# Kernel optimization log

Measured on AMD Instinct MI355X. Metric: run time of the kernel, lower is better.

Reference implementation:

```python
import jax, jax.numpy as jnp
import numpy as np
import math

B, M, N = 1, 128, 256
LIG_C = 256      # rep_1d num_c
ATTN_C = 32      # attention_num_c
HEADS = 8        # num_heads
EPS = 1e-5


def setup_inputs() -> dict:
    key = jax.random.key(0)
    ks = jax.random.split(key, 8)
    s = 1.0 / math.sqrt(LIG_C)
    return {
        "lig_profile": jax.random.normal(ks[0], (B, M, N, LIG_C), dtype=jnp.float32),
        "ln_scale": jnp.ones((LIG_C,), dtype=jnp.float32),
        "ln_bias": jnp.zeros((LIG_C,), dtype=jnp.float32),
        "wq": jax.random.normal(ks[1], (LIG_C, ATTN_C * HEADS), dtype=jnp.float32) * s,
        "wk": jax.random.normal(ks[2], (LIG_C, ATTN_C * HEADS), dtype=jnp.float32) * s,
        "wv": jax.random.normal(ks[3], (LIG_C, ATTN_C * HEADS), dtype=jnp.float32) * s,
        "wf": jax.random.normal(ks[4], (ATTN_C * HEADS, LIG_C), dtype=jnp.float32) * s,
        "bf": jnp.zeros((LIG_C,), dtype=jnp.float32),
    }


def reference(lig_profile, ln_scale, ln_bias, wq, wk, wv, wf, bf):
    # LayerNorm over channel dim
    mu = jnp.mean(lig_profile, axis=-1, keepdims=True)
    var = jnp.mean(jnp.square(lig_profile - mu), axis=-1, keepdims=True)
    x = (lig_profile - mu) * jax.lax.rsqrt(var + EPS) * ln_scale + ln_bias

    # QKV projections; view splits last dim as (attn_c, heads) -> channel-major layout
    shape5 = x.shape[:-1] + (ATTN_C, HEADS)
    q = (x @ wq).reshape(shape5)  # [b,m,n,c,h]
    k = (x @ wk).reshape(shape5)
    v = (x @ wv).reshape(shape5)

    factor = 1.0 / math.sqrt(ATTN_C)
    aff = jnp.einsum('bmich,bmjch->bmijh', q, k) * factor  # [b,m,i,j,h]
    weights = jax.nn.softmax(aff, axis=-2)                  # softmax over j (keys)
    out = jnp.einsum('bmrch,bmirh->bmich', v, weights)      # [b,m,i,c,h]
    out = out.reshape(out.shape[:-2] + (ATTN_C * HEADS,))
    return out @ wf + bf
```

## Files before the change

kernel.cpp:

```cpp
#include <hip/hip_runtime.h>

typedef _Float16 f16;
typedef _Float16 f16x8 __attribute__((ext_vector_type(8)));
typedef _Float16 f16x4 __attribute__((ext_vector_type(4)));
typedef _Float16 f16x2 __attribute__((ext_vector_type(2)));
typedef float f32x4 __attribute__((ext_vector_type(4)));
typedef float f32x16 __attribute__((ext_vector_type(16)));

#define MDIM 128
#define NDIM 256
#define CDIM 256
#define ROWS (MDIM*NDIM)

__device__ inline int pk2(float a, float b) {
  union { f16x2 h; int i; } u;
  u.h[0] = (f16)a; u.h[1] = (f16)b;
  return u.i;
}

__global__ __launch_bounds__(256) void k_prep(
    const float* __restrict__ wq, const float* __restrict__ wk,
    const float* __restrict__ wv, const float* __restrict__ wf,
    f16* __restrict__ bq, f16* __restrict__ bk, f16* __restrict__ bv,
    f16* __restrict__ bw)
{
  int idx   = blockIdx.x & 255;
  int which = blockIdx.x >> 8;
  int kk    = threadIdx.x;
  if (which < 3) {
    const float* W = which == 0 ? wq : which == 1 ? wk : wv;
    f16* dst       = which == 0 ? bq : which == 1 ? bk : bv;
    float sc = which == 0 ? (0.17677669529663689f * 1.4426950408889634f) : 1.0f;
    int j = (idx & 31) * 8 + (idx >> 5);
    dst[idx * 256 + kk] = (f16)(W[(size_t)kk * 256 + j] * sc);
  } else {
    int pkk = (kk & 31) * 8 + (kk >> 5);
    bw[idx * 256 + kk] = (f16)wf[(size_t)pkk * 256 + idx];
  }
}

__global__ __launch_bounds__(256) void k_lnqkv(const float* __restrict__ x,
    const float* __restrict__ g, const float* __restrict__ bb,
    const f16* __restrict__ bq, const f16* __restrict__ bk, const f16* __restrict__ bv,
    f16* __restrict__ qo, f16* __restrict__ ko, f16* __restrict__ vT)
{
  __shared__ f16 As[64][264];
  __shared__ f16 Bs[64][264];
  __shared__ f16 vtmp[64][72];
  int bm = blockIdx.x;
  int t = threadIdx.x, lane = t & 63, w = t >> 6;
  int wr = w >> 1, wc = w & 1;
  int l15 = lane & 15, l4 = lane >> 4;
  const float4 gv  = *(const float4*)(g + lane * 4);
  const float4 bv4 = *(const float4*)(bb + lane * 4);
#pragma unroll 4
  for (int rr = 0; rr < 16; ++rr) {
    int r = w * 16 + rr;
    const float4 xv = *(const float4*)(x + (size_t)(bm * 64 + r) * 256 + lane * 4);
    float s  = xv.x + xv.y + xv.z + xv.w;
    float s2 = xv.x*xv.x + xv.y*xv.y + xv.z*xv.z + xv.w*xv.w;
#pragma unroll
    for (int mm = 1; mm < 64; mm <<= 1) {
      s  += __shfl_xor(s,  mm, 64);
      s2 += __shfl_xor(s2, mm, 64);
    }
    float mu  = s * (1.0f / 256.0f);
    float var = s2 * (1.0f / 256.0f) - mu * mu;
    float rs  = rsqrtf(var + 1e-5f);
    f16x4 ov;
    ov[0] = (f16)((xv.x - mu) * rs * gv.x + bv4.x);
    ov[1] = (f16)((xv.y - mu) * rs * gv.y + bv4.y);
    ov[2] = (f16)((xv.z - mu) * rs * gv.z + bv4.z);
    ov[3] = (f16)((xv.w - mu) * rs * gv.w + bv4.w);
    *(f16x4*)&As[r][lane * 4] = ov;
  }
  for (int ct = 0; ct < 12; ++ct) {
    const f16* B = ct < 4 ? bq : ct < 8 ? bk : bv;
    int je0 = (ct & 3) * 64;
#pragma unroll
    for (int p = 0; p < 8; ++p) {
      int r = t >> 2, c0 = (t & 3) * 8 + p * 32;
      *(f16x8*)&Bs[r][c0] = *(const f16x8*)(B + (size_t)(je0 + r) * 256 + c0);
    }
    __syncthreads();
    f32x4 acc[2][2] = {};
#pragma unroll
    for (int kt = 0; kt < 8; ++kt) {
      f16x8 a0 = *(const f16x8*)&As[wr * 32 +      l15][kt * 32 + l4 * 8];
      f16x8 a1 = *(const f16x8*)&As[wr * 32 + 16 + l15][kt * 32 + l4 * 8];
      f16x8 b0 = *(const f16x8*)&Bs[wc * 32 +      l15][kt * 32 + l4 * 8];
      f16x8 b1 = *(const f16x8*)&Bs[wc * 32 + 16 + l15][kt * 32 + l4 * 8];
      acc[0][0] = __builtin_amdgcn_mfma_f32_16x16x32_f16(a0, b0, acc[0][0], 0, 0, 0);
      acc[0][1] = __builtin_amdgcn_mfma_f32_16x16x32_f16(a0, b1, acc[0][1], 0, 0, 0);
      acc[1][0] = __builtin_amdgcn_mfma_f32_16x16x32_f16(a1, b0, acc[1][0], 0, 0, 0);
      acc[1][1] = __builtin_amdgcn_mfma_f32_16x16x32_f16(a1, b1, acc[1][1], 0, 0, 0);
    }
    if (ct < 8) {
      f16* dst = ct < 4 ? qo : ko;
#pragma unroll
      for (int mi = 0; mi < 2; ++mi)
#pragma unroll
        for (int ni = 0; ni < 2; ++ni)
#pragma unroll
          for (int r = 0; r < 4; ++r) {
            int row = bm * 64 + wr * 32 + mi * 16 + l4 * 4 + r;
            int col = je0 + wc * 32 + ni * 16 + l15;
            dst[(size_t)row * 256 + col] = (f16)acc[mi][ni][r];
          }
    } else {
#pragma unroll
      for (int mi = 0; mi < 2; ++mi)
#pragma unroll
        for (int ni = 0; ni < 2; ++ni)
#pragma unroll
          for (int r = 0; r < 4; ++r)
            vtmp[wc * 32 + ni * 16 + l15][wr * 32 + mi * 16 + l4 * 4 + r] = (f16)acc[mi][ni][r];
      __syncthreads();
      int ch = t >> 2, np = (t & 3) * 16;
      size_t gdst = ((size_t)(bm >> 2) * 256 + je0 + ch) * 256 + (bm & 3) * 64 + np;
      *(f16x8*)(vT + gdst)     = *(const f16x8*)&vtmp[ch][np];
      *(f16x8*)(vT + gdst + 8) = *(const f16x8*)&vtmp[ch][np + 8];
    }
    __syncthreads();
  }
}

__global__ __launch_bounds__(256, 4) void k_attn(const f16* __restrict__ q,
    const f16* __restrict__ k, const f16* __restrict__ vT, f16* __restrict__ o)
{
  __shared__ f16 ks[256][40];
  __shared__ f16 vt[32][264];
  int bx = blockIdx.x;
  int m = bx >> 4, h = (bx >> 1) & 7, half = bx & 1;
  int t = threadIdx.x, lane = t & 63, w = t >> 6;
  int i32 = lane & 31, hi = lane >> 5;
  size_t rowbase = (size_t)m * 256;
#pragma unroll
  for (int p = 0; p < 4; ++p) {
    int n = p * 64 + (t >> 2);
    int c0 = (t & 3) * 8;
    *(f16x8*)&ks[n][c0] = *(const f16x8*)(k + (rowbase + n) * 256 + h * 32 + c0);
  }
#pragma unroll
  for (int p = 0; p < 4; ++p) {
    int idx = p * 256 + t;
    int c = idx >> 5, nb = (idx & 31) * 8;
    *(f16x8*)&vt[c][nb] = *(const f16x8*)(vT + ((size_t)m * 256 + h * 32 + c) * 256 + nb);
  }
  __syncthreads();
  int qi0 = half * 128 + w * 32;
  const f16* qp = q + (rowbase + qi0 + i32) * 256 + h * 32 + hi * 8;
  f16x8 qf0 = *(const f16x8*)(qp);
  f16x8 qf1 = *(const f16x8*)(qp + 16);
  f32x16 O = {};
  float m_run = -1e30f, l_run = 0.f;
#pragma unroll 2
  for (int kb = 0; kb < 8; ++kb) {
    f16x8 kf0 = *(const f16x8*)&ks[kb * 32 + i32][hi * 8];
    f16x8 kf1 = *(const f16x8*)&ks[kb * 32 + i32][16 + hi * 8];
    f32x16 s = {};
    s = __builtin_amdgcn_mfma_f32_32x32x16_f16(kf0, qf0, s, 0, 0, 0);
    s = __builtin_amdgcn_mfma_f32_32x32x16_f16(kf1, qf1, s, 0, 0, 0);
    float pmax = s[0];
#pragma unroll
    for (int r = 1; r < 16; ++r) pmax = fmaxf(pmax, s[r]);
    pmax = fmaxf(pmax, __shfl_xor(pmax, 32, 64));
    if (!__all(pmax - m_run <= 8.f)) {
      float m_new = fmaxf(m_run, pmax);
      float f = __builtin_amdgcn_exp2f(m_run - m_new);
      l_run *= f;
#pragma unroll
      for (int r = 0; r < 16; ++r)
        O[r] *= __shfl(f, (r & 3) + 8 * (r >> 2) + 4 * hi, 64);
      m_run = m_new;
    }
    float lsum = 0.f;
#pragma unroll
    for (int r = 0; r < 16; ++r) {
      float e = __builtin_amdgcn_exp2f(s[r] - m_run);
      s[r] = e;
      lsum += e;
    }
    lsum += __shfl_xor(lsum, 32, 64);
    l_run += lsum;
    int W0[4], W1[4];
#pragma unroll
    for (int qq = 0; qq < 4; ++qq) {
      W0[qq] = pk2(s[4 * qq],     s[4 * qq + 1]);
      W1[qq] = pk2(s[4 * qq + 2], s[4 * qq + 3]);
    }
#pragma unroll
    for (int ks2 = 0; ks2 < 2; ++ks2) {
      int X0 = W0[2 * ks2], Y0 = W0[2 * ks2 + 1];
      int X1 = W1[2 * ks2], Y1 = W1[2 * ks2 + 1];
      int a0 = __shfl(X0, i32, 64),      b0 = __shfl(Y0, i32, 64);
      int a1 = __shfl(X1, i32, 64),      b1 = __shfl(Y1, i32, 64);
      int a2 = __shfl(X0, i32 + 32, 64), b2 = __shfl(Y0, i32 + 32, 64);
      int a3 = __shfl(X1, i32 + 32, 64), b3 = __shfl(Y1, i32 + 32, 64);
      union { unsigned int ww[4]; f16x8 v; } pa;
      pa.ww[0] = hi ? (unsigned)b0 : (unsigned)a0;
      pa.ww[1] = hi ? (unsigned)b1 : (unsigned)a1;
      pa.ww[2] = hi ? (unsigned)b2 : (unsigned)a2;
      pa.ww[3] = hi ? (unsigned)b3 : (unsigned)a3;
      f16x8 vb = *(const f16x8*)&vt[i32][kb * 32 + ks2 * 16 + hi * 8];
      O = __builtin_amdgcn_mfma_f32_32x32x16_f16(pa.v, vb, O, 0, 0, 0);
    }
  }
  float inv = 1.f / l_run;
#pragma unroll
  for (int r = 0; r < 16; ++r) {
    int i = (r & 3) + 8 * (r >> 2) + 4 * hi;
    float fr = __shfl(inv, i, 64);
    o[(rowbase + (size_t)(qi0 + i)) * 256 + h * 32 + i32] = (f16)(O[r] * fr);
  }
}

__global__ __launch_bounds__(256) void k_out(const f16* __restrict__ a,
    const f16* __restrict__ bw, const float* __restrict__ bias,
    float* __restrict__ out)
{
  __shared__ f16 As[64][264];
  __shared__ f16 Bs[64][264];
  int bm = blockIdx.x;
  int t = threadIdx.x, lane = t & 63, w = t >> 6;
  int wr = w >> 1, wc = w & 1;
  int l15 = lane & 15, l4 = lane >> 4;
#pragma unroll
  for (int p = 0; p < 8; ++p) {
    int r = t >> 2, c0 = (t & 3) * 8 + p * 32;
    *(f16x8*)&As[r][c0] = *(const f16x8*)(a + (size_t)(bm * 64 + r) * 256 + c0);
  }
  for (int ct = 0; ct < 4; ++ct) {
    int col0 = ct * 64;
#pragma unroll
    for (int p = 0; p < 8; ++p) {
      int r = t >> 2, c0 = (t & 3) * 8 + p * 32;
      *(f16x8*)&Bs[r][c0] = *(const f16x8*)(bw + (size_t)(col0 + r) * 256 + c0);
    }
    __syncthreads();
    f32x4 acc[2][2] = {};
#pragma unroll
    for (int kt = 0; kt < 8; ++kt) {
      f16x8 a0 = *(const f16x8*)&As[wr * 32 +      l15][kt * 32 + l4 * 8];
      f16x8 a1 = *(const f16x8*)&As[wr * 32 + 16 + l15][kt * 32 + l4 * 8];
      f16x8 b0 = *(const f16x8*)&Bs[wc * 32 +      l15][kt * 32 + l4 * 8];
      f16x8 b1 = *(const f16x8*)&Bs[wc * 32 + 16 + l15][kt * 32 + l4 * 8];
      acc[0][0] = __builtin_amdgcn_mfma_f32_16x16x32_f16(a0, b0, acc[0][0], 0, 0, 0);
      acc[0][1] = __builtin_amdgcn_mfma_f32_16x16x32_f16(a0, b1, acc[0][1], 0, 0, 0);
      acc[1][0] = __builtin_amdgcn_mfma_f32_16x16x32_f16(a1, b0, acc[1][0], 0, 0, 0);
      acc[1][1] = __builtin_amdgcn_mfma_f32_16x16x32_f16(a1, b1, acc[1][1], 0, 0, 0);
    }
#pragma unroll
    for (int mi = 0; mi < 2; ++mi)
#pragma unroll
      for (int ni = 0; ni < 2; ++ni)
#pragma unroll
        for (int r = 0; r < 4; ++r) {
          int row = bm * 64 + wr * 32 + mi * 16 + l4 * 4 + r;
          int col = col0 + wc * 32 + ni * 16 + l15;
          out[(size_t)row * 256 + col] = acc[mi][ni][r] + bias[col];
        }
    __syncthreads();
  }
}

extern "C" void kernel_launch(void* const* d_in, const int* in_sizes, int n_in,
                              void* d_out, int out_size, void* d_ws, size_t ws_size,
                              hipStream_t stream)
{
  const float* x  = (const float*)d_in[0];
  const float* g  = (const float*)d_in[1];
  const float* b  = (const float*)d_in[2];
  const float* wq = (const float*)d_in[3];
  const float* wk = (const float*)d_in[4];
  const float* wv = (const float*)d_in[5];
  const float* wf = (const float*)d_in[6];
  const float* bf = (const float*)d_in[7];
  float* out = (float*)d_out;

  char* ws = (char*)d_ws;
  f16* ah  = (f16*)(ws);
  f16* qh  = (f16*)(ws + (size_t)16 * 1024 * 1024);
  f16* kh  = (f16*)(ws + (size_t)32 * 1024 * 1024);
  f16* vTh = (f16*)(ws + (size_t)48 * 1024 * 1024);
  char* wbase = ws + (size_t)64 * 1024 * 1024;
  f16* bq = (f16*)(wbase);
  f16* bk = (f16*)(wbase + 128 * 1024);
  f16* bv = (f16*)(wbase + 256 * 1024);
  f16* bw = (f16*)(wbase + 384 * 1024);

  k_prep <<<1024, 256, 0, stream>>>(wq, wk, wv, wf, bq, bk, bv, bw);
  k_lnqkv<<<512,  256, 0, stream>>>(x, g, b, bq, bk, bv, qh, kh, vTh);
  k_attn <<<2048, 256, 0, stream>>>(qh, kh, vTh, ah);
  k_out  <<<512,  256, 0, stream>>>(ah, bw, bf, out);
}
```

Measured before the change: 84.05 us.

## Prefetch GEMM weight tiles, merge attention halves, add MFMA priority, coalesce weight prep

The weight-prep kernel now transposes through LDS with coalesced reads and vectorized writes, using only 16 blocks. The QKV and output GEMMs register-prefetch the next weight tile while the current one is computed. Attention merges the two query halves into one 512-thread block so K/V are loaded once per (m,h), and wraps the MFMAs with s_setprio. The log2e factor moves from the Q weights to a per-score multiply. These are meant to cut redundant K/V loads and hide global-load latency, at the cost of extra VALU work and more register pressure. A 16-block prep kernel also leaves most CUs idle.

```diff
diff --git a/kernel.cpp b/kernel.cpp
--- a/kernel.cpp
+++ b/kernel.cpp
@@ -11,6 +11,7 @@
 #define NDIM 256
 #define CDIM 256
 #define ROWS (MDIM*NDIM)
+#define L2E 1.4426950408889634f
 
 __device__ inline int pk2(float a, float b) {
   union { f16x2 h; int i; } u;
@@ -24,18 +25,39 @@
     f16* __restrict__ bq, f16* __restrict__ bk, f16* __restrict__ bv,
     f16* __restrict__ bw)
 {
-  int idx   = blockIdx.x & 255;
-  int which = blockIdx.x >> 8;
-  int kk    = threadIdx.x;
+  __shared__ f16 ld[64][264];
+  int which = blockIdx.x >> 2, kb = blockIdx.x & 3;
+  int t = threadIdx.x;
+  int k0 = kb * 64;
   if (which < 3) {
     const float* W = which == 0 ? wq : which == 1 ? wk : wv;
     f16* dst       = which == 0 ? bq : which == 1 ? bk : bv;
-    float sc = which == 0 ? (0.17677669529663689f * 1.4426950408889634f) : 1.0f;
-    int j = (idx & 31) * 8 + (idx >> 5);
-    dst[idx * 256 + kk] = (f16)(W[(size_t)kk * 256 + j] * sc);
+    float sc = which == 0 ? 0.17677669529663689f : 1.0f;
+    for (int r = 0; r < 64; ++r)
+      ld[r][t] = (f16)(W[(size_t)(k0 + r) * 256 + t] * sc);
+    __syncthreads();
+    int j = (t & 31) * 8 + (t >> 5);
+#pragma unroll
+    for (int rr = 0; rr < 8; ++rr) {
+      f16x8 o;
+#pragma unroll
+      for (int i = 0; i < 8; ++i) o[i] = ld[rr * 8 + i][j];
+      *(f16x8*)(dst + (size_t)t * 256 + k0 + rr * 8) = o;
+    }
   } else {
-    int pkk = (kk & 31) * 8 + (kk >> 5);
-    bw[idx * 256 + kk] = (f16)wf[(size_t)pkk * 256 + idx];
+    for (int r = 0; r < 64; ++r) {
+      int ke = k0 + r;
+      int jr = (ke & 31) * 8 + (ke >> 5);
+      ld[r][t] = (f16)wf[(size_t)jr * 256 + t];
+    }
+    __syncthreads();
+#pragma unroll
+    for (int rr = 0; rr < 8; ++rr) {
+      f16x8 o;
+#pragma unroll
+      for (int i = 0; i < 8; ++i) o[i] = ld[rr * 8 + i][t];
+      *(f16x8*)(bw + (size_t)t * 256 + k0 + rr * 8) = o;
+    }
   }
 }
 
@@ -51,6 +73,11 @@
   int t = threadIdx.x, lane = t & 63, w = t >> 6;
   int wr = w >> 1, wc = w & 1;
   int l15 = lane & 15, l4 = lane >> 4;
+  int pr = t >> 2, pc = (t & 3) * 8;
+  f16x8 pf[8];
+#pragma unroll
+  for (int p = 0; p < 8; ++p)
+    pf[p] = *(const f16x8*)(bq + (size_t)pr * 256 + pc + p * 32);
   const float4 gv  = *(const float4*)(g + lane * 4);
   const float4 bv4 = *(const float4*)(bb + lane * 4);
 #pragma unroll 4
@@ -75,14 +102,18 @@
     *(f16x4*)&As[r][lane * 4] = ov;
   }
   for (int ct = 0; ct < 12; ++ct) {
-    const f16* B = ct < 4 ? bq : ct < 8 ? bk : bv;
     int je0 = (ct & 3) * 64;
 #pragma unroll
-    for (int p = 0; p < 8; ++p) {
-      int r = t >> 2, c0 = (t & 3) * 8 + p * 32;
-      *(f16x8*)&Bs[r][c0] = *(const f16x8*)(B + (size_t)(je0 + r) * 256 + c0);
-    }
-    __syncthreads();
+    for (int p = 0; p < 8; ++p)
+      *(f16x8*)&Bs[pr][pc + p * 32] = pf[p];
+    __syncthreads();
+    if (ct < 11) {
+      const f16* Bn = (ct + 1) < 4 ? bq : (ct + 1) < 8 ? bk : bv;
+      int je0n = ((ct + 1) & 3) * 64;
+#pragma unroll
+      for (int p = 0; p < 8; ++p)
+        pf[p] = *(const f16x8*)(Bn + (size_t)(je0n + pr) * 256 + pc + p * 32);
+    }
     f32x4 acc[2][2] = {};
 #pragma unroll
     for (int kt = 0; kt < 8; ++kt) {
@@ -125,30 +156,30 @@
   }
 }
 
-__global__ __launch_bounds__(256, 4) void k_attn(const f16* __restrict__ q,
+__global__ __launch_bounds__(512, 4) void k_attn(const f16* __restrict__ q,
     const f16* __restrict__ k, const f16* __restrict__ vT, f16* __restrict__ o)
 {
   __shared__ f16 ks[256][40];
   __shared__ f16 vt[32][264];
   int bx = blockIdx.x;
-  int m = bx >> 4, h = (bx >> 1) & 7, half = bx & 1;
+  int m = bx >> 3, h = bx & 7;
   int t = threadIdx.x, lane = t & 63, w = t >> 6;
   int i32 = lane & 31, hi = lane >> 5;
   size_t rowbase = (size_t)m * 256;
 #pragma unroll
-  for (int p = 0; p < 4; ++p) {
-    int n = p * 64 + (t >> 2);
+  for (int p = 0; p < 2; ++p) {
+    int n = p * 128 + (t >> 2);
     int c0 = (t & 3) * 8;
     *(f16x8*)&ks[n][c0] = *(const f16x8*)(k + (rowbase + n) * 256 + h * 32 + c0);
   }
 #pragma unroll
-  for (int p = 0; p < 4; ++p) {
-    int idx = p * 256 + t;
+  for (int p = 0; p < 2; ++p) {
+    int idx = p * 512 + t;
     int c = idx >> 5, nb = (idx & 31) * 8;
     *(f16x8*)&vt[c][nb] = *(const f16x8*)(vT + ((size_t)m * 256 + h * 32 + c) * 256 + nb);
   }
   __syncthreads();
-  int qi0 = half * 128 + w * 32;
+  int qi0 = w * 32;
   const f16* qp = q + (rowbase + qi0 + i32) * 256 + h * 32 + hi * 8;
   f16x8 qf0 = *(const f16x8*)(qp);
   f16x8 qf1 = *(const f16x8*)(qp + 16);
@@ -159,8 +190,12 @@
     f16x8 kf0 = *(const f16x8*)&ks[kb * 32 + i32][hi * 8];
     f16x8 kf1 = *(const f16x8*)&ks[kb * 32 + i32][16 + hi * 8];
     f32x16 s = {};
+    __builtin_amdgcn_s_setprio(1);
     s = __builtin_amdgcn_mfma_f32_32x32x16_f16(kf0, qf0, s, 0, 0, 0);
     s = __builtin_amdgcn_mfma_f32_32x32x16_f16(kf1, qf1, s, 0, 0, 0);
+    __builtin_amdgcn_s_setprio(0);
+#pragma unroll
+    for (int r = 0; r < 16; ++r) s[r] *= L2E;
     float pmax = s[0];
 #pragma unroll
     for (int r = 1; r < 16; ++r) pmax = fmaxf(pmax, s[r]);
@@ -203,7 +238,9 @@
       pa.ww[2] = hi ? (unsigned)b2 : (unsigned)a2;
       pa.ww[3] = hi ? (unsigned)b3 : (unsigned)a3;
       f16x8 vb = *(const f16x8*)&vt[i32][kb * 32 + ks2 * 16 + hi * 8];
+      __builtin_amdgcn_s_setprio(1);
       O = __builtin_amdgcn_mfma_f32_32x32x16_f16(pa.v, vb, O, 0, 0, 0);
+      __builtin_amdgcn_s_setprio(0);
     }
   }
   float inv = 1.f / l_run;
@@ -225,19 +262,25 @@
   int t = threadIdx.x, lane = t & 63, w = t >> 6;
   int wr = w >> 1, wc = w & 1;
   int l15 = lane & 15, l4 = lane >> 4;
-#pragma unroll
-  for (int p = 0; p < 8; ++p) {
-    int r = t >> 2, c0 = (t & 3) * 8 + p * 32;
-    *(f16x8*)&As[r][c0] = *(const f16x8*)(a + (size_t)(bm * 64 + r) * 256 + c0);
-  }
+  int pr = t >> 2, pc = (t & 3) * 8;
+  f16x8 pf[8];
+#pragma unroll
+  for (int p = 0; p < 8; ++p)
+    pf[p] = *(const f16x8*)(bw + (size_t)pr * 256 + pc + p * 32);
+#pragma unroll
+  for (int p = 0; p < 8; ++p)
+    *(f16x8*)&As[pr][pc + p * 32] = *(const f16x8*)(a + (size_t)(bm * 64 + pr) * 256 + pc + p * 32);
   for (int ct = 0; ct < 4; ++ct) {
     int col0 = ct * 64;
 #pragma unroll
-    for (int p = 0; p < 8; ++p) {
-      int r = t >> 2, c0 = (t & 3) * 8 + p * 32;
-      *(f16x8*)&Bs[r][c0] = *(const f16x8*)(bw + (size_t)(col0 + r) * 256 + c0);
-    }
-    __syncthreads();
+    for (int p = 0; p < 8; ++p)
+      *(f16x8*)&Bs[pr][pc + p * 32] = pf[p];
+    __syncthreads();
+    if (ct < 3) {
+#pragma unroll
+      for (int p = 0; p < 8; ++p)
+        pf[p] = *(const f16x8*)(bw + (size_t)((ct + 1) * 64 + pr) * 256 + pc + p * 32);
+    }
     f32x4 acc[2][2] = {};
 #pragma unroll
     for (int kt = 0; kt < 8; ++kt) {
@@ -289,8 +332,8 @@
   f16* bv = (f16*)(wbase + 256 * 1024);
   f16* bw = (f16*)(wbase + 384 * 1024);
 
-  k_prep <<<1024, 256, 0, stream>>>(wq, wk, wv, wf, bq, bk, bv, bw);
+  k_prep <<<16,   256, 0, stream>>>(wq, wk, wv, wf, bq, bk, bv, bw);
   k_lnqkv<<<512,  256, 0, stream>>>(x, g, b, bq, bk, bv, qh, kh, vTh);
-  k_attn <<<2048, 256, 0, stream>>>(qh, kh, vTh, ah);
+  k_attn <<<1024, 512, 0, stream>>>(qh, kh, vTh, ah);
   k_out  <<<512,  256, 0, stream>>>(ah, bw, bf, out);
 }
```

Measured after the change: 82.23 us. 1.02x faster.
